# Kernel tuning notes

Measured on AMD Instinct MI355X. Metric: run time of the kernel, lower is better.

## Reference

```python
import jax, jax.numpy as jnp
import numpy as np

B = 256          # graphs per batch
N = 128          # nodes per graph (equal-size graphs; batch is block-contiguous)
P = N * (N - 1) // 2  # pairs per graph = 8128
E = B * 1024     # total edges
D = 128          # node feature dim
L = 32           # latent dim

# precomputed local upper-triangular pair indices (constants)
_PI, _PJ = np.triu_indices(N, k=1)
_PI = jnp.asarray(_PI); _PJ = jnp.asarray(_PJ)


def setup_inputs() -> dict:
    key = jax.random.key(0)
    ks = jax.random.split(key, 8)
    x = jax.random.normal(ks[0], (B * N, D), dtype=jnp.float32)
    # within-graph edges with local i < j
    li = jax.random.randint(ks[1], (E,), 0, N - 1)
    r = jax.random.randint(ks[2], (E,), 0, 1 << 30)
    lj = li + 1 + r % (N - 1 - li)
    g = jax.random.randint(ks[3], (E,), 0, B)
    off = g * N
    edge_index = jnp.stack([off + li, off + lj]).astype(jnp.int64)
    batch = jnp.repeat(jnp.arange(B), N).astype(jnp.int64)
    eps = jax.random.normal(ks[4], (B * N, L), dtype=jnp.float32)
    W1 = jax.random.normal(ks[5], (D, D), dtype=jnp.float32) * 0.05
    b1 = jnp.zeros((D,), dtype=jnp.float32)
    Wmu = jax.random.normal(ks[6], (D, L), dtype=jnp.float32) * 0.05
    bmu = jnp.zeros((L,), dtype=jnp.float32)
    Wls = jax.random.normal(ks[7], (D, L), dtype=jnp.float32) * 0.05
    bls = jnp.zeros((L,), dtype=jnp.float32)
    return {"x": x, "edge_index": edge_index, "batch": batch, "eps": eps,
            "W1": W1, "b1": b1, "Wmu": Wmu, "bmu": bmu, "Wls": Wls, "bls": bls}


def reference(x, edge_index, batch, eps, W1, b1, Wmu, bmu, Wls, bls):
    src, dst = edge_index[0], edge_index[1]
    # --- encoder: one symmetric message-passing layer -> Gaussian q per node ---
    agg = jnp.zeros_like(x).at[dst].add(x[src]).at[src].add(x[dst])
    h = jax.nn.relu((x + agg) @ W1 + b1)
    mu = h @ Wmu + bmu                       # [BN, L]
    log_std = h @ Wls + bls
    std = jnp.exp(log_std)
    z = mu + std * eps                       # rsample
    # --- KL(q || N(0,I)) per node, summed per graph (kls[b]) ---
    kl_node = 0.5 * jnp.sum(std * std + mu * mu - 1.0 - 2.0 * log_std, axis=-1)
    kls = jax.ops.segment_sum(kl_node, batch, num_segments=B)  # [B]
    # --- link targets: scatter edges into triangular pair slots ---
    li, lj, be = src % N, dst % N, src // N
    pidx = li * (2 * N - li - 1) // 2 + (lj - li - 1)
    targets = jnp.zeros((B, P), dtype=z.dtype).at[be, pidx].set(1.0)
    # --- inner-product Bernoulli decoder over all pairs of every graph ---
    zb = z.reshape(B, N, L)
    logits = jnp.einsum('bpl,bpl->bp', zb[:, _PI], zb[:, _PJ])   # [B, P]
    log_probs = jnp.sum(targets * logits - jax.nn.softplus(logits), axis=-1)  # [B]
    elbo = jnp.mean(log_probs - kls)
    return -elbo
```

## Files before the change

### kernel.cpp

```cpp
#include <hip/hip_runtime.h>
#include <math.h>

#define B_ 256
#define N_ 128
#define D_ 128
#define L_ 32
#define E_ 262144
#define PW_ 254
#define DCAP 96

#define NDEG_OFF 0
#define BM_OFF   32768
#define KLS_OFF  97792
#define LP_OFF   98048
#define ADJ_OFF  98304
#define Z_OFF    884736
#define ZERO_WORDS 98304

__global__ __launch_bounds__(256) void k_build(
    const int* __restrict__ ei, unsigned* __restrict__ ndeg,
    unsigned char* __restrict__ adj, unsigned* __restrict__ bm)
{
    int e = blockIdx.x * 256 + threadIdx.x;
    int src = ei[e], dst = ei[E_ + e];
    unsigned s1 = atomicAdd(&ndeg[src], 1u);
    if (s1 < DCAP) adj[(size_t)src * DCAP + s1] = (unsigned char)(dst & 127);
    unsigned s2 = atomicAdd(&ndeg[dst], 1u);
    if (s2 < DCAP) adj[(size_t)dst * DCAP + s2] = (unsigned char)(src & 127);
    int li = src & 127, lj = dst & 127, g = src >> 7;
    int p = li * (255 - li) / 2 + (lj - li - 1);
    atomicOr(&bm[g * PW_ + (p >> 5)], 1u << (p & 31));
}

__global__ __launch_bounds__(256) void k_encoder(
    const float* __restrict__ x, const unsigned* __restrict__ ndeg,
    const unsigned char* __restrict__ adj,
    const float* __restrict__ W1, const float* __restrict__ b1,
    const float* __restrict__ Wmu, const float* __restrict__ bmu,
    const float* __restrict__ Wls, const float* __restrict__ bls,
    const float* __restrict__ eps,
    float* __restrict__ z, float* __restrict__ kls)
{
    __shared__ float XAs[64 * 132];
    __shared__ float Ws[4096];
    __shared__ float RED[256];
    int t = threadIdx.x;
    int row0 = blockIdx.x * 64;
    int g = blockIdx.x >> 1;
    int ty = t >> 4, tx = t & 15;

    {
        int nidx = t >> 5;
        int fo = (t & 31) << 2;
        #pragma unroll 2
        for (int p = 0; p < 8; ++p) {
            int lrow = p * 8 + nidx;
            int gnode = row0 + lrow;
            const float* xr = x + (size_t)gnode * 128 + fo;
            float4 acc = *(const float4*)xr;
            int deg = (int)ndeg[gnode];
            if (deg > DCAP) deg = DCAP;
            const unsigned char* al = adj + (size_t)gnode * DCAP;
            const float* gx = x + (size_t)(gnode & ~127) * 128 + fo;
            int e = 0;
            for (; e + 4 <= deg; e += 4) {
                unsigned pk = *(const unsigned*)(al + e);
                float4 v0 = *(const float4*)(gx + (pk & 255u) * 128);
                float4 v1 = *(const float4*)(gx + ((pk >> 8) & 255u) * 128);
                float4 v2 = *(const float4*)(gx + ((pk >> 16) & 255u) * 128);
                float4 v3 = *(const float4*)(gx + (pk >> 24) * 128);
                acc.x += v0.x + v1.x + v2.x + v3.x;
                acc.y += v0.y + v1.y + v2.y + v3.y;
                acc.z += v0.z + v1.z + v2.z + v3.z;
                acc.w += v0.w + v1.w + v2.w + v3.w;
            }
            for (; e < deg; ++e) {
                float4 v = *(const float4*)(gx + (unsigned)al[e] * 128);
                acc.x += v.x; acc.y += v.y; acc.z += v.z; acc.w += v.w;
            }
            *(float4*)(XAs + lrow * 132 + fo) = acc;
        }
    }
    __syncthreads();

    float acc[4][8];
    #pragma unroll
    for (int i = 0; i < 4; ++i)
        #pragma unroll
        for (int j = 0; j < 8; ++j) acc[i][j] = 0.f;

    for (int kq = 0; kq < 4; ++kq) {
        if (kq) __syncthreads();
        #pragma unroll
        for (int i = 0; i < 4; ++i) {
            int c = t + i * 256;
            ((float4*)Ws)[c] = ((const float4*)(W1 + kq * 4096))[c];
        }
        __syncthreads();
        #pragma unroll 4
        for (int k = 0; k < 32; ++k) {
            int kk = kq * 32 + k;
            float a0 = XAs[(4 * ty + 0) * 132 + kk];
            float a1 = XAs[(4 * ty + 1) * 132 + kk];
            float a2 = XAs[(4 * ty + 2) * 132 + kk];
            float a3 = XAs[(4 * ty + 3) * 132 + kk];
            float4 w0 = *(const float4*)(Ws + k * 128 + 8 * tx);
            float4 w1 = *(const float4*)(Ws + k * 128 + 8 * tx + 4);
            float av[4] = {a0, a1, a2, a3};
            float wv[8] = {w0.x, w0.y, w0.z, w0.w, w1.x, w1.y, w1.z, w1.w};
            #pragma unroll
            for (int i = 0; i < 4; ++i)
                #pragma unroll
                for (int j = 0; j < 8; ++j) acc[i][j] += av[i] * wv[j];
        }
    }
    __syncthreads();

    {
        float4 bb0 = *(const float4*)(b1 + 8 * tx);
        float4 bb1 = *(const float4*)(b1 + 8 * tx + 4);
        float bb[8] = {bb0.x, bb0.y, bb0.z, bb0.w, bb1.x, bb1.y, bb1.z, bb1.w};
        #pragma unroll
        for (int i = 0; i < 4; ++i) {
            float4 h0, h1;
            h0.x = fmaxf(acc[i][0] + bb[0], 0.f);
            h0.y = fmaxf(acc[i][1] + bb[1], 0.f);
            h0.z = fmaxf(acc[i][2] + bb[2], 0.f);
            h0.w = fmaxf(acc[i][3] + bb[3], 0.f);
            h1.x = fmaxf(acc[i][4] + bb[4], 0.f);
            h1.y = fmaxf(acc[i][5] + bb[5], 0.f);
            h1.z = fmaxf(acc[i][6] + bb[6], 0.f);
            h1.w = fmaxf(acc[i][7] + bb[7], 0.f);
            *(float4*)(XAs + (4 * ty + i) * 132 + 8 * tx)     = h0;
            *(float4*)(XAs + (4 * ty + i) * 132 + 8 * tx + 4) = h1;
        }
    }

    float a2c[4][4];
    #pragma unroll
    for (int i = 0; i < 4; ++i)
        #pragma unroll
        for (int j = 0; j < 4; ++j) a2c[i][j] = 0.f;

    for (int kh = 0; kh < 2; ++kh) {
        __syncthreads();
        #pragma unroll
        for (int i = 0; i < 4; ++i) {
            int c = t + i * 256;
            int row = (c >> 4) + kh * 64, col4 = (c & 15) << 2;
            float4 v = (col4 < 32) ? *(const float4*)(Wmu + row * 32 + col4)
                                   : *(const float4*)(Wls + row * 32 + col4 - 32);
            *(float4*)(Ws + (c >> 4) * 64 + col4) = v;
        }
        __syncthreads();
        #pragma unroll 4
        for (int k = 0; k < 64; ++k) {
            int kk = kh * 64 + k;
            float h0 = XAs[(4 * ty + 0) * 132 + kk];
            float h1 = XAs[(4 * ty + 1) * 132 + kk];
            float h2 = XAs[(4 * ty + 2) * 132 + kk];
            float h3 = XAs[(4 * ty + 3) * 132 + kk];
            float4 wv = *(const float4*)(Ws + k * 64 + 4 * tx);
            float hv[4] = {h0, h1, h2, h3};
            float wa[4] = {wv.x, wv.y, wv.z, wv.w};
            #pragma unroll
            for (int i = 0; i < 4; ++i)
                #pragma unroll
                for (int j = 0; j < 4; ++j) a2c[i][j] += hv[i] * wa[j];
        }
    }
    {
        float4 bv = (tx < 8) ? *(const float4*)(bmu + 4 * tx)
                             : *(const float4*)(bls + 4 * (tx - 8));
        float ba[4] = {bv.x, bv.y, bv.z, bv.w};
        #pragma unroll
        for (int i = 0; i < 4; ++i)
            #pragma unroll
            for (int j = 0; j < 4; ++j) a2c[i][j] += ba[j];
    }
    float oth[4][4];
    #pragma unroll
    for (int i = 0; i < 4; ++i)
        #pragma unroll
        for (int j = 0; j < 4; ++j) oth[i][j] = __shfl_xor(a2c[i][j], 8);

    float klsum = 0.f;
    {
        int i0 = (tx < 8) ? 0 : 2;
        int l0 = 4 * (tx & 7);
        #pragma unroll
        for (int ii = 0; ii < 2; ++ii) {
            int i = i0 + ii;
            int rowg = row0 + 4 * ty + i;
            float mu[4], lsv[4];
            #pragma unroll
            for (int j = 0; j < 4; ++j) {
                mu[j]  = (tx < 8) ? a2c[i][j] : oth[i][j];
                lsv[j] = (tx < 8) ? oth[i][j] : a2c[i][j];
            }
            float4 ev = *(const float4*)(eps + (size_t)rowg * 32 + l0);
            float ea[4] = {ev.x, ev.y, ev.z, ev.w};
            float4 zv;
            float zz[4];
            #pragma unroll
            for (int j = 0; j < 4; ++j) {
                float s = expf(lsv[j]);
                zz[j] = mu[j] + s * ea[j];
                klsum += s * s + mu[j] * mu[j] - 1.f - 2.f * lsv[j];
            }
            zv.x = zz[0]; zv.y = zz[1]; zv.z = zz[2]; zv.w = zz[3];
            *(float4*)(z + (size_t)rowg * 32 + l0) = zv;
        }
    }
    RED[t] = klsum;
    __syncthreads();
    for (int s = 128; s > 0; s >>= 1) {
        if (t < s) RED[t] += RED[t + s];
        __syncthreads();
    }
    if (t == 0) atomicAdd(&kls[g], 0.5f * RED[0]);
}

__global__ __launch_bounds__(256) void k_decoder(
    const float* __restrict__ z, const unsigned* __restrict__ bitmap,
    float* __restrict__ logp)
{
    __shared__ float zT[32 * 132];
    __shared__ unsigned bm[PW_];
    __shared__ float RED[256];
    int b = blockIdx.x >> 1, half = blockIdx.x & 1, t = threadIdx.x;

    #pragma unroll
    for (int i = 0; i < 16; ++i) {
        int c = t + i * 256;
        int n = c >> 5, l = c & 31;
        zT[l * 132 + n] = z[((size_t)b * N_ + n) * L_ + l];
    }
    if (t < PW_) bm[t] = bitmap[b * PW_ + t];
    __syncthreads();

    int i0 = half * 64 + ((t >> 5) << 3);
    int j0 = (t & 31) << 2;
    float g[8][4];
    #pragma unroll
    for (int a = 0; a < 8; ++a)
        #pragma unroll
        for (int c = 0; c < 4; ++c) g[a][c] = 0.f;

    #pragma unroll 4
    for (int l = 0; l < 32; ++l) {
        float4 a0 = *(const float4*)(zT + l * 132 + i0);
        float4 a1 = *(const float4*)(zT + l * 132 + i0 + 4);
        float4 b0 = *(const float4*)(zT + l * 132 + j0);
        float za[8] = {a0.x, a0.y, a0.z, a0.w, a1.x, a1.y, a1.z, a1.w};
        float zb[4] = {b0.x, b0.y, b0.z, b0.w};
        #pragma unroll
        for (int a = 0; a < 8; ++a)
            #pragma unroll
            for (int c = 0; c < 4; ++c) g[a][c] += za[a] * zb[c];
    }

    float sum = 0.f;
    #pragma unroll
    for (int a = 0; a < 8; ++a) {
        int i = i0 + a;
        #pragma unroll
        for (int c = 0; c < 4; ++c) {
            int j = j0 + c;
            if (j > i) {
                float lg = g[a][c];
                int p = i * (255 - i) / 2 + (j - i - 1);
                unsigned bit = (bm[p >> 5] >> (p & 31)) & 1u;
                float sp = log1pf(expf(-fabsf(lg))) + fmaxf(lg, 0.f);
                sum += bit ? (lg - sp) : (-sp);
            }
        }
    }
    RED[t] = sum;
    __syncthreads();
    for (int s = 128; s > 0; s >>= 1) {
        if (t < s) RED[t] += RED[t + s];
        __syncthreads();
    }
    if (t == 0) atomicAdd(&logp[b], RED[0]);
}

__global__ __launch_bounds__(256) void k_finalize(
    const float* __restrict__ kls, const float* __restrict__ logp,
    float* __restrict__ out)
{
    __shared__ float RED[256];
    int t = threadIdx.x;
    RED[t] = logp[t] - kls[t];
    __syncthreads();
    for (int s = 128; s > 0; s >>= 1) {
        if (t < s) RED[t] += RED[t + s];
        __syncthreads();
    }
    if (t == 0) out[0] = -RED[0] * (1.0f / 256.0f);
}

extern "C" void kernel_launch(void* const* d_in, const int* in_sizes, int n_in,
                              void* d_out, int out_size, void* d_ws, size_t ws_size,
                              hipStream_t stream) {
    const float* x   = (const float*)d_in[0];
    const int*   ei  = (const int*)d_in[1];
    const float* eps = (const float*)d_in[3];
    const float* W1  = (const float*)d_in[4];
    const float* b1  = (const float*)d_in[5];
    const float* Wmu = (const float*)d_in[6];
    const float* bmu = (const float*)d_in[7];
    const float* Wls = (const float*)d_in[8];
    const float* bls = (const float*)d_in[9];

    unsigned* wsw = (unsigned*)d_ws;
    unsigned*      ndeg = wsw + NDEG_OFF;
    unsigned*      bm   = wsw + BM_OFF;
    float*         kls  = (float*)(wsw + KLS_OFF);
    float*         logp = (float*)(wsw + LP_OFF);
    unsigned char* adj  = (unsigned char*)(wsw + ADJ_OFF);
    float*         z    = (float*)(wsw + Z_OFF);

    hipMemsetAsync(d_ws, 0, ZERO_WORDS * sizeof(unsigned), stream);

    k_build   <<<E_ / 256, 256, 0, stream>>>(ei, ndeg, adj, bm);
    k_encoder <<<512, 256, 0, stream>>>(x, ndeg, adj, W1, b1, Wmu, bmu,
                                        Wls, bls, eps, z, kls);
    k_decoder <<<2 * B_, 256, 0, stream>>>(z, bm, logp);
    k_finalize<<<1, 256, 0, stream>>>(kls, logp, (float*)d_out);
}
```

Before: 209.4 us.

## Halve rows per block in encoder and decoder to double grid size

The encoder now processes 32 nodes per block instead of 64 and launches 1024 blocks, with a new thread mapping: 8-wide feature gathers, float4 k-chunked GEMM tiles, and a 4x2 output tile for the mu/log_std projection. The decoder splits each graph into four quarters instead of two and launches 1024 blocks with a 4x4 register tile. The aim is more blocks and occupancy (launch bounds min 4) on the many-CU GPU, at the cost of redundant W1 and z staging per block and more kls atomics.

```diff
diff --git a/kernel.cpp b/kernel.cpp
--- a/kernel.cpp
+++ b/kernel.cpp
@@ -32,7 +32,7 @@
     atomicOr(&bm[g * PW_ + (p >> 5)], 1u << (p & 31));
 }
 
-__global__ __launch_bounds__(256) void k_encoder(
+__global__ __launch_bounds__(256, 4) void k_encoder(
     const float* __restrict__ x, const unsigned* __restrict__ ndeg,
     const unsigned char* __restrict__ adj,
     const float* __restrict__ W1, const float* __restrict__ b1,
@@ -41,23 +41,24 @@
     const float* __restrict__ eps,
     float* __restrict__ z, float* __restrict__ kls)
 {
-    __shared__ float XAs[64 * 132];
+    __shared__ float XAs[32 * 132];
     __shared__ float Ws[4096];
     __shared__ float RED[256];
     int t = threadIdx.x;
-    int row0 = blockIdx.x * 64;
-    int g = blockIdx.x >> 1;
-    int ty = t >> 4, tx = t & 15;
+    int row0 = blockIdx.x * 32;
+    int g = blockIdx.x >> 2;
+    int rg = t >> 5;
+    int cg = t & 31;
 
     {
-        int nidx = t >> 5;
-        int fo = (t & 31) << 2;
-        #pragma unroll 2
-        for (int p = 0; p < 8; ++p) {
-            int lrow = p * 8 + nidx;
+        int nidx = t >> 4;
+        int fo = (t & 15) * 8;
+        for (int p = 0; p < 2; ++p) {
+            int lrow = p * 16 + nidx;
             int gnode = row0 + lrow;
             const float* xr = x + (size_t)gnode * 128 + fo;
-            float4 acc = *(const float4*)xr;
+            float4 a0 = *(const float4*)xr;
+            float4 a1 = *(const float4*)(xr + 4);
             int deg = (int)ndeg[gnode];
             if (deg > DCAP) deg = DCAP;
             const unsigned char* al = adj + (size_t)gnode * DCAP;
@@ -65,29 +66,40 @@
             int e = 0;
             for (; e + 4 <= deg; e += 4) {
                 unsigned pk = *(const unsigned*)(al + e);
-                float4 v0 = *(const float4*)(gx + (pk & 255u) * 128);
-                float4 v1 = *(const float4*)(gx + ((pk >> 8) & 255u) * 128);
-                float4 v2 = *(const float4*)(gx + ((pk >> 16) & 255u) * 128);
-                float4 v3 = *(const float4*)(gx + (pk >> 24) * 128);
-                acc.x += v0.x + v1.x + v2.x + v3.x;
-                acc.y += v0.y + v1.y + v2.y + v3.y;
-                acc.z += v0.z + v1.z + v2.z + v3.z;
-                acc.w += v0.w + v1.w + v2.w + v3.w;
+                const float* r0 = gx + (pk & 255u) * 128;
+                const float* r1 = gx + ((pk >> 8) & 255u) * 128;
+                const float* r2 = gx + ((pk >> 16) & 255u) * 128;
+                const float* r3 = gx + (pk >> 24) * 128;
+                float4 v00 = *(const float4*)r0, v01 = *(const float4*)(r0 + 4);
+                float4 v10 = *(const float4*)r1, v11 = *(const float4*)(r1 + 4);
+                float4 v20 = *(const float4*)r2, v21 = *(const float4*)(r2 + 4);
+                float4 v30 = *(const float4*)r3, v31 = *(const float4*)(r3 + 4);
+                a0.x += v00.x + v10.x + v20.x + v30.x;
+                a0.y += v00.y + v10.y + v20.y + v30.y;
+                a0.z += v00.z + v10.z + v20.z + v30.z;
+                a0.w += v00.w + v10.w + v20.w + v30.w;
+                a1.x += v01.x + v11.x + v21.x + v31.x;
+                a1.y += v01.y + v11.y + v21.y + v31.y;
+                a1.z += v01.z + v11.z + v21.z + v31.z;
+                a1.w += v01.w + v11.w + v21.w + v31.w;
             }
             for (; e < deg; ++e) {
-                float4 v = *(const float4*)(gx + (unsigned)al[e] * 128);
-                acc.x += v.x; acc.y += v.y; acc.z += v.z; acc.w += v.w;
-            }
-            *(float4*)(XAs + lrow * 132 + fo) = acc;
-        }
-    }
-    __syncthreads();
-
-    float acc[4][8];
+                const float* r = gx + (unsigned)al[e] * 128;
+                float4 v0 = *(const float4*)r, v1 = *(const float4*)(r + 4);
+                a0.x += v0.x; a0.y += v0.y; a0.z += v0.z; a0.w += v0.w;
+                a1.x += v1.x; a1.y += v1.y; a1.z += v1.z; a1.w += v1.w;
+            }
+            *(float4*)(XAs + lrow * 132 + fo) = a0;
+            *(float4*)(XAs + lrow * 132 + fo + 4) = a1;
+        }
+    }
+    __syncthreads();
+
+    float acc[4][4];
     #pragma unroll
     for (int i = 0; i < 4; ++i)
         #pragma unroll
-        for (int j = 0; j < 8; ++j) acc[i][j] = 0.f;
+        for (int j = 0; j < 4; ++j) acc[i][j] = 0.f;
 
     for (int kq = 0; kq < 4; ++kq) {
         if (kq) __syncthreads();
@@ -97,119 +109,100 @@
             ((float4*)Ws)[c] = ((const float4*)(W1 + kq * 4096))[c];
         }
         __syncthreads();
-        #pragma unroll 4
-        for (int k = 0; k < 32; ++k) {
-            int kk = kq * 32 + k;
-            float a0 = XAs[(4 * ty + 0) * 132 + kk];
-            float a1 = XAs[(4 * ty + 1) * 132 + kk];
-            float a2 = XAs[(4 * ty + 2) * 132 + kk];
-            float a3 = XAs[(4 * ty + 3) * 132 + kk];
-            float4 w0 = *(const float4*)(Ws + k * 128 + 8 * tx);
-            float4 w1 = *(const float4*)(Ws + k * 128 + 8 * tx + 4);
-            float av[4] = {a0, a1, a2, a3};
-            float wv[8] = {w0.x, w0.y, w0.z, w0.w, w1.x, w1.y, w1.z, w1.w};
+        #pragma unroll 2
+        for (int k = 0; k < 32; k += 4) {
+            float4 av[4], wv[4];
             #pragma unroll
             for (int i = 0; i < 4; ++i)
-                #pragma unroll
-                for (int j = 0; j < 8; ++j) acc[i][j] += av[i] * wv[j];
+                av[i] = *(const float4*)(XAs + (4 * rg + i) * 132 + kq * 32 + k);
+            #pragma unroll
+            for (int dk = 0; dk < 4; ++dk)
+                wv[dk] = *(const float4*)(Ws + (k + dk) * 128 + 4 * cg);
+            #pragma unroll
+            for (int i = 0; i < 4; ++i) {
+                acc[i][0] += av[i].x * wv[0].x + av[i].y * wv[1].x + av[i].z * wv[2].x + av[i].w * wv[3].x;
+                acc[i][1] += av[i].x * wv[0].y + av[i].y * wv[1].y + av[i].z * wv[2].y + av[i].w * wv[3].y;
+                acc[i][2] += av[i].x * wv[0].z + av[i].y * wv[1].z + av[i].z * wv[2].z + av[i].w * wv[3].z;
+                acc[i][3] += av[i].x * wv[0].w + av[i].y * wv[1].w + av[i].z * wv[2].w + av[i].w * wv[3].w;
+            }
         }
     }
     __syncthreads();
 
     {
-        float4 bb0 = *(const float4*)(b1 + 8 * tx);
-        float4 bb1 = *(const float4*)(b1 + 8 * tx + 4);
-        float bb[8] = {bb0.x, bb0.y, bb0.z, bb0.w, bb1.x, bb1.y, bb1.z, bb1.w};
+        float4 bb = *(const float4*)(b1 + 4 * cg);
         #pragma unroll
         for (int i = 0; i < 4; ++i) {
-            float4 h0, h1;
-            h0.x = fmaxf(acc[i][0] + bb[0], 0.f);
-            h0.y = fmaxf(acc[i][1] + bb[1], 0.f);
-            h0.z = fmaxf(acc[i][2] + bb[2], 0.f);
-            h0.w = fmaxf(acc[i][3] + bb[3], 0.f);
-            h1.x = fmaxf(acc[i][4] + bb[4], 0.f);
-            h1.y = fmaxf(acc[i][5] + bb[5], 0.f);
-            h1.z = fmaxf(acc[i][6] + bb[6], 0.f);
-            h1.w = fmaxf(acc[i][7] + bb[7], 0.f);
-            *(float4*)(XAs + (4 * ty + i) * 132 + 8 * tx)     = h0;
-            *(float4*)(XAs + (4 * ty + i) * 132 + 8 * tx + 4) = h1;
-        }
-    }
-
-    float a2c[4][4];
-    #pragma unroll
-    for (int i = 0; i < 4; ++i)
-        #pragma unroll
-        for (int j = 0; j < 4; ++j) a2c[i][j] = 0.f;
+            float4 h;
+            h.x = fmaxf(acc[i][0] + bb.x, 0.f);
+            h.y = fmaxf(acc[i][1] + bb.y, 0.f);
+            h.z = fmaxf(acc[i][2] + bb.z, 0.f);
+            h.w = fmaxf(acc[i][3] + bb.w, 0.f);
+            *(float4*)(XAs + (4 * rg + i) * 132 + 4 * cg) = h;
+        }
+    }
+
+    float a3[4][2];
+    #pragma unroll
+    for (int i = 0; i < 4; ++i) { a3[i][0] = 0.f; a3[i][1] = 0.f; }
 
     for (int kh = 0; kh < 2; ++kh) {
         __syncthreads();
         #pragma unroll
         for (int i = 0; i < 4; ++i) {
             int c = t + i * 256;
-            int row = (c >> 4) + kh * 64, col4 = (c & 15) << 2;
-            float4 v = (col4 < 32) ? *(const float4*)(Wmu + row * 32 + col4)
-                                   : *(const float4*)(Wls + row * 32 + col4 - 32);
-            *(float4*)(Ws + (c >> 4) * 64 + col4) = v;
-        }
-        __syncthreads();
-        #pragma unroll 4
-        for (int k = 0; k < 64; ++k) {
-            int kk = kh * 64 + k;
-            float h0 = XAs[(4 * ty + 0) * 132 + kk];
-            float h1 = XAs[(4 * ty + 1) * 132 + kk];
-            float h2 = XAs[(4 * ty + 2) * 132 + kk];
-            float h3 = XAs[(4 * ty + 3) * 132 + kk];
-            float4 wv = *(const float4*)(Ws + k * 64 + 4 * tx);
-            float hv[4] = {h0, h1, h2, h3};
-            float wa[4] = {wv.x, wv.y, wv.z, wv.w};
+            int row = c >> 4, col4 = (c & 15) << 2;
+            int rowg = kh * 64 + row;
+            float4 v = (col4 < 32) ? *(const float4*)(Wmu + rowg * 32 + col4)
+                                   : *(const float4*)(Wls + rowg * 32 + col4 - 32);
+            *(float4*)(Ws + row * 64 + col4) = v;
+        }
+        __syncthreads();
+        #pragma unroll 2
+        for (int k = 0; k < 64; k += 4) {
+            float4 av[4];
+            float2 wv[4];
             #pragma unroll
             for (int i = 0; i < 4; ++i)
-                #pragma unroll
-                for (int j = 0; j < 4; ++j) a2c[i][j] += hv[i] * wa[j];
+                av[i] = *(const float4*)(XAs + (4 * rg + i) * 132 + kh * 64 + k);
+            #pragma unroll
+            for (int dk = 0; dk < 4; ++dk)
+                wv[dk] = *(const float2*)(Ws + (k + dk) * 64 + 2 * cg);
+            #pragma unroll
+            for (int i = 0; i < 4; ++i) {
+                a3[i][0] += av[i].x * wv[0].x + av[i].y * wv[1].x + av[i].z * wv[2].x + av[i].w * wv[3].x;
+                a3[i][1] += av[i].x * wv[0].y + av[i].y * wv[1].y + av[i].z * wv[2].y + av[i].w * wv[3].y;
+            }
         }
     }
     {
-        float4 bv = (tx < 8) ? *(const float4*)(bmu + 4 * tx)
-                             : *(const float4*)(bls + 4 * (tx - 8));
-        float ba[4] = {bv.x, bv.y, bv.z, bv.w};
-        #pragma unroll
-        for (int i = 0; i < 4; ++i)
-            #pragma unroll
-            for (int j = 0; j < 4; ++j) a2c[i][j] += ba[j];
-    }
-    float oth[4][4];
-    #pragma unroll
-    for (int i = 0; i < 4; ++i)
-        #pragma unroll
-        for (int j = 0; j < 4; ++j) oth[i][j] = __shfl_xor(a2c[i][j], 8);
+        float2 bv = (cg < 16) ? *(const float2*)(bmu + 2 * cg)
+                              : *(const float2*)(bls + 2 * cg - 32);
+        #pragma unroll
+        for (int i = 0; i < 4; ++i) { a3[i][0] += bv.x; a3[i][1] += bv.y; }
+    }
+
+    float o3[4][2];
+    #pragma unroll
+    for (int i = 0; i < 4; ++i) {
+        o3[i][0] = __shfl_xor(a3[i][0], 16);
+        o3[i][1] = __shfl_xor(a3[i][1], 16);
+    }
 
     float klsum = 0.f;
-    {
-        int i0 = (tx < 8) ? 0 : 2;
-        int l0 = 4 * (tx & 7);
-        #pragma unroll
-        for (int ii = 0; ii < 2; ++ii) {
-            int i = i0 + ii;
-            int rowg = row0 + 4 * ty + i;
-            float mu[4], lsv[4];
-            #pragma unroll
-            for (int j = 0; j < 4; ++j) {
-                mu[j]  = (tx < 8) ? a2c[i][j] : oth[i][j];
-                lsv[j] = (tx < 8) ? oth[i][j] : a2c[i][j];
-            }
-            float4 ev = *(const float4*)(eps + (size_t)rowg * 32 + l0);
-            float ea[4] = {ev.x, ev.y, ev.z, ev.w};
-            float4 zv;
-            float zz[4];
-            #pragma unroll
-            for (int j = 0; j < 4; ++j) {
-                float s = expf(lsv[j]);
-                zz[j] = mu[j] + s * ea[j];
-                klsum += s * s + mu[j] * mu[j] - 1.f - 2.f * lsv[j];
-            }
-            zv.x = zz[0]; zv.y = zz[1]; zv.z = zz[2]; zv.w = zz[3];
-            *(float4*)(z + (size_t)rowg * 32 + l0) = zv;
+    if (cg < 16) {
+        int lo = cg;
+        #pragma unroll
+        for (int i = 0; i < 4; ++i) {
+            int rowg = row0 + 4 * rg + i;
+            float mu0 = a3[i][0], mu1 = a3[i][1];
+            float ls0 = o3[i][0], ls1 = o3[i][1];
+            float2 ev = *(const float2*)(eps + (size_t)rowg * 32 + 2 * lo);
+            float s0 = expf(ls0), s1 = expf(ls1);
+            float2 zv = make_float2(mu0 + s0 * ev.x, mu1 + s1 * ev.y);
+            *(float2*)(z + (size_t)rowg * 32 + 2 * lo) = zv;
+            klsum += s0 * s0 + mu0 * mu0 - 1.f - 2.f * ls0
+                   + s1 * s1 + mu1 * mu1 - 1.f - 2.f * ls1;
         }
     }
     RED[t] = klsum;
@@ -228,7 +221,7 @@
     __shared__ float zT[32 * 132];
     __shared__ unsigned bm[PW_];
     __shared__ float RED[256];
-    int b = blockIdx.x >> 1, half = blockIdx.x & 1, t = threadIdx.x;
+    int b = blockIdx.x >> 2, quar = blockIdx.x & 3, t = threadIdx.x;
 
     #pragma unroll
     for (int i = 0; i < 16; ++i) {
@@ -239,30 +232,29 @@
     if (t < PW_) bm[t] = bitmap[b * PW_ + t];
     __syncthreads();
 
-    int i0 = half * 64 + ((t >> 5) << 3);
+    int i0 = quar * 32 + ((t >> 5) << 2);
     int j0 = (t & 31) << 2;
-    float g[8][4];
-    #pragma unroll
-    for (int a = 0; a < 8; ++a)
+    float g[4][4];
+    #pragma unroll
+    for (int a = 0; a < 4; ++a)
         #pragma unroll
         for (int c = 0; c < 4; ++c) g[a][c] = 0.f;
 
     #pragma unroll 4
     for (int l = 0; l < 32; ++l) {
         float4 a0 = *(const float4*)(zT + l * 132 + i0);
-        float4 a1 = *(const float4*)(zT + l * 132 + i0 + 4);
         float4 b0 = *(const float4*)(zT + l * 132 + j0);
-        float za[8] = {a0.x, a0.y, a0.z, a0.w, a1.x, a1.y, a1.z, a1.w};
+        float za[4] = {a0.x, a0.y, a0.z, a0.w};
         float zb[4] = {b0.x, b0.y, b0.z, b0.w};
         #pragma unroll
-        for (int a = 0; a < 8; ++a)
+        for (int a = 0; a < 4; ++a)
             #pragma unroll
             for (int c = 0; c < 4; ++c) g[a][c] += za[a] * zb[c];
     }
 
     float sum = 0.f;
     #pragma unroll
-    for (int a = 0; a < 8; ++a) {
+    for (int a = 0; a < 4; ++a) {
         int i = i0 + a;
         #pragma unroll
         for (int c = 0; c < 4; ++c) {
@@ -324,8 +316,8 @@
     hipMemsetAsync(d_ws, 0, ZERO_WORDS * sizeof(unsigned), stream);
 
     k_build   <<<E_ / 256, 256, 0, stream>>>(ei, ndeg, adj, bm);
-    k_encoder <<<512, 256, 0, stream>>>(x, ndeg, adj, W1, b1, Wmu, bmu,
-                                        Wls, bls, eps, z, kls);
-    k_decoder <<<2 * B_, 256, 0, stream>>>(z, bm, logp);
+    k_encoder <<<1024, 256, 0, stream>>>(x, ndeg, adj, W1, b1, Wmu, bmu,
+                                         Wls, bls, eps, z, kls);
+    k_decoder <<<4 * B_, 256, 0, stream>>>(z, bm, logp);
     k_finalize<<<1, 256, 0, stream>>>(kls, logp, (float*)d_out);
 }
```

Result: faster. 201.1 us (-4.0%).
